# Kernel optimization log

Measured on AMD Instinct MI355X. Metric: run time of the kernel, lower is better.

The kernel has to match this reference:

```python
import jax, jax.numpy as jnp
import numpy as np

N, E, H, D, L = 50000, 800000, 4, 128, 4
HD = H * D  # 512
NEG_SLOPE_ATTN = 0.2   # DGL GATConv leaky_relu on attention logits
NEG_SLOPE_ACT = 0.01   # F.leaky_relu activation on output
LN_EPS = 1e-5

def _leaky(x, s):
    return jnp.where(x > 0, x, s * x)

def setup_inputs() -> dict:
    key = jax.random.key(0)
    ks = jax.random.split(key, 12)
    features = jax.random.normal(ks[0], (N, D), dtype=jnp.float32)
    src = jax.random.randint(ks[1], (E,), 0, N, dtype=jnp.int32)
    dst = jax.random.randint(ks[2], (E,), 0, N, dtype=jnp.int32)
    s = 0.05
    W_fc   = jax.random.normal(ks[3], (L, D, HD), dtype=jnp.float32) * s
    attn_l = jax.random.normal(ks[4], (L, H, D), dtype=jnp.float32) * s
    attn_r = jax.random.normal(ks[5], (L, H, D), dtype=jnp.float32) * s
    W_res  = jax.random.normal(ks[6], (L, D, HD), dtype=jnp.float32) * s
    b_gat  = jnp.zeros((L, HD), dtype=jnp.float32)
    W_nrm  = jax.random.normal(ks[7], (L, HD, D), dtype=jnp.float32) * s
    b_nrm  = jnp.zeros((L, D), dtype=jnp.float32)
    ln_g   = jnp.ones((L, D), dtype=jnp.float32)
    ln_b   = jnp.zeros((L, D), dtype=jnp.float32)
    return dict(features=features, src=src, dst=dst, W_fc=W_fc, attn_l=attn_l,
                attn_r=attn_r, W_res=W_res, b_gat=b_gat, W_nrm=W_nrm,
                b_nrm=b_nrm, ln_g=ln_g, ln_b=ln_b)

def _gat_layer(x, src, dst, Wf, al, ar, Wr, b):
    feat = (x @ Wf).reshape(N, H, D)                      # [N,H,D]
    el = jnp.einsum('nhd,hd->nh', feat, al)               # [N,H]
    er = jnp.einsum('nhd,hd->nh', feat, ar)
    e = _leaky(el[src] + er[dst], NEG_SLOPE_ATTN)         # [E,H]
    m = jax.ops.segment_max(e, dst, num_segments=N)       # segment softmax over in-edges
    ex = jnp.exp(e - m[dst])
    z = jax.ops.segment_sum(ex, dst, num_segments=N)
    alpha = ex / jnp.maximum(z[dst], 1e-20)               # [E,H]
    msg = feat[src] * alpha[:, :, None]                   # [E,H,D] (dominant traffic)
    rst = jax.ops.segment_sum(msg, dst, num_segments=N)   # [N,H,D]
    rst = rst + (x @ Wr).reshape(N, H, D)                 # linear residual
    rst = rst + b.reshape(H, D)
    rst = _leaky(rst, NEG_SLOPE_ACT)                      # activation
    return rst.reshape(N, HD)

def _layernorm(y, g, b):
    mu = jnp.mean(y, axis=-1, keepdims=True)
    var = jnp.mean(jnp.square(y - mu), axis=-1, keepdims=True)
    return (y - mu) * jax.lax.rsqrt(var + LN_EPS) * g + b

def reference(features, src, dst, W_fc, attn_l, attn_r, W_res, b_gat, W_nrm, b_nrm, ln_g, ln_b):
    x = features
    for l in range(L):
        h = _gat_layer(x, src, dst, W_fc[l], attn_l[l], attn_r[l], W_res[l], b_gat[l])
        y = h @ W_nrm[l] + b_nrm[l]
        x = _layernorm(y, ln_g[l], ln_b[l])
    return x
```

## Files before the change

kernel.cpp:

```cpp
#include <hip/hip_runtime.h>
#include <math.h>

#define NN 50000
#define NPAD 50048
#define EE 800000
#define HH 4
#define DD 128
#define HDIM 512
#define LL 4

typedef __attribute__((ext_vector_type(8))) short short8;
typedef __attribute__((ext_vector_type(4))) float f32x4;

__device__ __forceinline__ float lk(float x, float s){ return x > 0.f ? x : s*x; }
__device__ __forceinline__ unsigned short f2bf(float f){
  unsigned u = __float_as_uint(f);
  u += 0x7FFFu + ((u >> 16) & 1u);
  return (unsigned short)(u >> 16);
}
__device__ __forceinline__ float lo16(unsigned u){ return __uint_as_float(u << 16); }
__device__ __forceinline__ float hi16(unsigned u){ return __uint_as_float(u & 0xFFFF0000u); }

__global__ void k_zero(int* p, int n){ int i = blockIdx.x*blockDim.x+threadIdx.x; if(i<n) p[i]=0; }

__global__ void k_hist(const int* __restrict__ dst, int* __restrict__ cnt){
  int e = blockIdx.x*blockDim.x+threadIdx.x;
  if (e < EE) atomicAdd(&cnt[dst[e]], 1);
}

__global__ __launch_bounds__(1024) void k_scan(const int* __restrict__ cnt, int* __restrict__ row_ptr){
  __shared__ int part[1024];
  int t = threadIdx.x;
  const int chunk = (NN + 1023)/1024;
  int b = t*chunk, e = b+chunk;
  if (b > NN) b = NN;
  if (e > NN) e = NN;
  int s = 0;
  for (int i=b;i<e;++i) s += cnt[i];
  part[t] = s;
  __syncthreads();
  for (int off=1; off<1024; off<<=1){
    int v = (t>=off) ? part[t-off] : 0;
    __syncthreads();
    part[t] += v;
    __syncthreads();
  }
  int run = part[t] - s;
  for (int i=b;i<e;++i){ row_ptr[i] = run; run += cnt[i]; }
  if (t==1023) row_ptr[NN] = part[1023];
}

__global__ void k_copy(const int* __restrict__ a, int* __restrict__ b, int n){
  int i = blockIdx.x*blockDim.x+threadIdx.x; if(i<n) b[i]=a[i];
}

__global__ void k_fill(const int* __restrict__ src, const int* __restrict__ dst,
                       int* __restrict__ cursor, int* __restrict__ csr_src){
  int e = blockIdx.x*blockDim.x+threadIdx.x;
  if (e >= EE) return;
  int d = dst[e];
  int p = atomicAdd(&cursor[d], 1);
  csr_src[p] = src[e];
}

__global__ __launch_bounds__(256) void k_cvtw2(const float* __restrict__ Wf,
                                               const float* __restrict__ Wr,
                                               unsigned short* __restrict__ W2t){
  __shared__ float tile[64][65];
  int t = threadIdx.x;
  int n0 = blockIdx.x*64, k0 = blockIdx.y*64, l = blockIdx.z;
  const float* srcp = (n0 < 512) ? Wf : Wr;
  int nsrc = (n0 < 512) ? n0 : (n0 - 512);
  #pragma unroll
  for (int j=0;j<16;++j){
    int idx = t + j*256; int kk = idx>>6, nn = idx&63;
    tile[kk][nn] = srcp[(size_t)(l*128 + k0+kk)*512 + nsrc+nn];
  }
  __syncthreads();
  #pragma unroll
  for (int j=0;j<16;++j){
    int idx = t + j*256; int nn = idx>>6, kk = idx&63;
    W2t[((size_t)l*1024 + n0+nn)*128 + k0+kk] = f2bf(tile[kk][nn]);
  }
}
__global__ __launch_bounds__(256) void k_cvtwn(const float* __restrict__ Wn,
                                               unsigned short* __restrict__ Wnt){
  __shared__ float tile[64][65];
  int t = threadIdx.x;
  int n0 = blockIdx.x*64, k0 = blockIdx.y*64, l = blockIdx.z;
  #pragma unroll
  for (int j=0;j<16;++j){
    int idx = t + j*256; int kk = idx>>6, nn = idx&63;
    tile[kk][nn] = Wn[(size_t)(l*512 + k0+kk)*128 + n0+nn];
  }
  __syncthreads();
  #pragma unroll
  for (int j=0;j<16;++j){
    int idx = t + j*256; int nn = idx>>6, kk = idx&63;
    Wnt[((size_t)l*128 + n0+nn)*512 + k0+kk] = f2bf(tile[kk][nn]);
  }
}
__global__ void k_cvtx(const float* __restrict__ x, unsigned short* __restrict__ xb){
  int idx = blockIdx.x*blockDim.x + threadIdx.x;
  int row = idx >> 7;
  xb[idx] = (row < NN) ? f2bf(x[idx]) : (unsigned short)0;
}

__global__ __launch_bounds__(256) void k_gemm1m(const unsigned short* __restrict__ xb,
                                                const unsigned short* __restrict__ W2t,
                                                const float* __restrict__ al,
                                                const float* __restrict__ ar,
                                                unsigned char* __restrict__ featQ,
                                                unsigned short* __restrict__ hbuf,
                                                float2* __restrict__ elsc,
                                                float* __restrict__ erp){
  __shared__ __attribute__((aligned(16))) char smem[2*128*136*2];
  __shared__ float sAl[128], sAr[128];
  __shared__ float sInv[128];
  unsigned short* sA = (unsigned short*)smem;
  unsigned short* sB = sA + 128*136;
  int t = threadIdx.x;
  int m0 = blockIdx.x*128;
  int n0 = blockIdx.y*128;
  int h = n0 >> 7;
  if (n0 < 512 && t < 128){ sAl[t] = al[h*128 + t]; sAr[t] = ar[h*128 + t]; }
  #pragma unroll
  for (int j=0;j<8;++j){
    int c = t + j*256; int r = c>>4, kc = c&15;
    uint4 v = *(const uint4*)(xb + (size_t)(m0+r)*128 + kc*8);
    *(uint4*)(sA + r*136 + kc*8) = v;
  }
  #pragma unroll
  for (int j=0;j<8;++j){
    int c = t + j*256; int r = c>>4, kc = c&15;
    uint4 v = *(const uint4*)(W2t + (size_t)(n0+r)*128 + kc*8);
    *(uint4*)(sB + r*136 + kc*8) = v;
  }
  __syncthreads();

  int lane = t & 63, w = t >> 6;
  int wm = (w & 1)*64, wn = (w >> 1)*64;
  int lrow = lane & 15, quad = lane >> 4;
  f32x4 acc[4][4];
  #pragma unroll
  for (int mt=0;mt<4;++mt)
    #pragma unroll
    for (int nt=0;nt<4;++nt) acc[mt][nt] = (f32x4){0.f,0.f,0.f,0.f};

  #pragma unroll
  for (int kq=0;kq<4;++kq){
    int kb = kq*32 + quad*8;
    short8 af[4], bf[4];
    #pragma unroll
    for (int mt=0;mt<4;++mt) af[mt] = *(const short8*)(sA + (wm+mt*16+lrow)*136 + kb);
    #pragma unroll
    for (int nt=0;nt<4;++nt) bf[nt] = *(const short8*)(sB + (wn+nt*16+lrow)*136 + kb);
    #pragma unroll
    for (int mt=0;mt<4;++mt)
      #pragma unroll
      for (int nt=0;nt<4;++nt)
        acc[mt][nt] = __builtin_amdgcn_mfma_f32_16x16x32_bf16(af[mt], bf[nt], acc[mt][nt], 0,0,0);
  }

  __syncthreads();
  #pragma unroll
  for (int mt=0;mt<4;++mt)
    #pragma unroll
    for (int nt=0;nt<4;++nt)
      #pragma unroll
      for (int r=0;r<4;++r)
        sA[(wm+mt*16+quad*4+r)*136 + wn+nt*16+lrow] = f2bf(acc[mt][nt][r]);
  __syncthreads();

  if (n0 >= 512){
    unsigned short* dstB = hbuf + (size_t)m0*512 + (n0-512);
    #pragma unroll
    for (int j=0;j<8;++j){
      int c = t + j*256; int r = c>>4, kc = c&15;
      uint4 v = *(const uint4*)(sA + r*136 + kc*8);
      *(uint4*)(dstB + (size_t)r*512 + kc*8) = v;
    }
  } else {
    int r = t >> 1, half = t & 1;
    int base = half*64;
    float accl = 0.f, accr = 0.f, amax = 0.f;
    #pragma unroll
    for (int d=0; d<64; d+=4){
      uint2 u = *(const uint2*)&sA[r*136 + base + d];
      float f0=lo16(u.x), f1=hi16(u.x), f2=lo16(u.y), f3=hi16(u.y);
      float4 a  = *(const float4*)&sAl[base+d];
      float4 rr = *(const float4*)&sAr[base+d];
      accl += f0*a.x + f1*a.y + f2*a.z + f3*a.w;
      accr += f0*rr.x + f1*rr.y + f2*rr.z + f3*rr.w;
      amax = fmaxf(amax, fmaxf(fmaxf(fabsf(f0), fabsf(f1)), fmaxf(fabsf(f2), fabsf(f3))));
    }
    accl += __shfl_xor(accl, 1);
    accr += __shfl_xor(accr, 1);
    amax = fmaxf(amax, __shfl_xor(amax, 1));
    float am = fmaxf(amax, 1e-8f);
    if (half == 0){
      sInv[r] = 127.f / am;
      if ((m0+r) < NN){
        elsc[(size_t)(m0+r)*4 + h] = make_float2(accl, am * (1.f/127.f));
        erp[(size_t)(m0+r)*4 + h] = accr;
      }
    }
    __syncthreads();
    float qinv = sInv[r];
    unsigned char* qdst = featQ + (size_t)(m0+r)*512 + n0 + base;
    #pragma unroll
    for (int g=0; g<4; ++g){
      uint4 ua = *(const uint4*)&sA[r*136 + base + g*16];
      uint4 ub = *(const uint4*)&sA[r*136 + base + g*16 + 8];
      unsigned vals[8] = {ua.x, ua.y, ua.z, ua.w, ub.x, ub.y, ub.z, ub.w};
      unsigned p[4];
      #pragma unroll
      for (int j=0;j<4;++j){
        unsigned vlo = vals[2*j], vhi = vals[2*j+1];
        int q0 = (int)rintf(lo16(vlo)*qinv) + 128;
        int q1 = (int)rintf(hi16(vlo)*qinv) + 128;
        int q2 = (int)rintf(lo16(vhi)*qinv) + 128;
        int q3 = (int)rintf(hi16(vhi)*qinv) + 128;
        p[j] = (unsigned)q0 | ((unsigned)q1<<8) | ((unsigned)q2<<16) | ((unsigned)q3<<24);
      }
      *(uint4*)(qdst + g*16) = make_uint4(p[0],p[1],p[2],p[3]);
    }
  }
}

__global__ __launch_bounds__(256) void k_agg(const unsigned char* __restrict__ featQ,
                                             unsigned short* __restrict__ hbuf,
                                             const float2* __restrict__ elsc,
                                             const float* __restrict__ er,
                                             const int* __restrict__ row_ptr,
                                             const int* __restrict__ csr_src,
                                             const float* __restrict__ b_gat){
  int t = threadIdx.x;
  int lane = t & 63;
  int node = blockIdx.x*4 + (t>>6);
  int beg = row_ptr[node], end = row_ptr[node+1];
  int hd = lane >> 4;
  float erh = er[(size_t)node*4 + hd];

  float z = 0.f, sws = 0.f;
  float a0=0.f,a1=0.f,a2=0.f,a3=0.f,a4=0.f,a5=0.f,a6=0.f,a7=0.f;
  const uint2* fQ = (const uint2*)featQ;

  int i = beg;
  for (; i + 3 < end; i += 4){
    int s0 = csr_src[i], s1 = csr_src[i+1], s2 = csr_src[i+2], s3 = csr_src[i+3];
    float2 q0 = elsc[(size_t)s0*4 + hd];
    float2 q1 = elsc[(size_t)s1*4 + hd];
    float2 q2 = elsc[(size_t)s2*4 + hd];
    float2 q3 = elsc[(size_t)s3*4 + hd];
    uint2 f0 = fQ[(size_t)s0*64 + lane];
    uint2 f1 = fQ[(size_t)s1*64 + lane];
    uint2 f2 = fQ[(size_t)s2*64 + lane];
    uint2 f3 = fQ[(size_t)s3*64 + lane];
    float w0 = __expf(lk(q0.x + erh, 0.2f));
    float w1 = __expf(lk(q1.x + erh, 0.2f));
    float w2 = __expf(lk(q2.x + erh, 0.2f));
    float w3 = __expf(lk(q3.x + erh, 0.2f));
    float ws0 = w0*q0.y, ws1 = w1*q1.y, ws2 = w2*q2.y, ws3 = w3*q3.y;
    z += w0 + w1 + w2 + w3;
    sws += ws0 + ws1 + ws2 + ws3;
    a0 += ws0*(float)(f0.x & 255u)      + ws1*(float)(f1.x & 255u)      + ws2*(float)(f2.x & 255u)      + ws3*(float)(f3.x & 255u);
    a1 += ws0*(float)((f0.x>>8) & 255u) + ws1*(float)((f1.x>>8) & 255u) + ws2*(float)((f2.x>>8) & 255u) + ws3*(float)((f3.x>>8) & 255u);
    a2 += ws0*(float)((f0.x>>16)& 255u) + ws1*(float)((f1.x>>16)& 255u) + ws2*(float)((f2.x>>16)& 255u) + ws3*(float)((f3.x>>16)& 255u);
    a3 += ws0*(float)(f0.x>>24)         + ws1*(float)(f1.x>>24)         + ws2*(float)(f2.x>>24)         + ws3*(float)(f3.x>>24);
    a4 += ws0*(float)(f0.y & 255u)      + ws1*(float)(f1.y & 255u)      + ws2*(float)(f2.y & 255u)      + ws3*(float)(f3.y & 255u);
    a5 += ws0*(float)((f0.y>>8) & 255u) + ws1*(float)((f1.y>>8) & 255u) + ws2*(float)((f2.y>>8) & 255u) + ws3*(float)((f3.y>>8) & 255u);
    a6 += ws0*(float)((f0.y>>16)& 255u) + ws1*(float)((f1.y>>16)& 255u) + ws2*(float)((f2.y>>16)& 255u) + ws3*(float)((f3.y>>16)& 255u);
    a7 += ws0*(float)(f0.y>>24)         + ws1*(float)(f1.y>>24)         + ws2*(float)(f2.y>>24)         + ws3*(float)(f3.y>>24);
  }
  for (; i < end; ++i){
    int s = csr_src[i];
    float2 q = elsc[(size_t)s*4 + hd];
    uint2 f = fQ[(size_t)s*64 + lane];
    float w = __expf(lk(q.x + erh, 0.2f));
    float ws = w*q.y;
    z += w; sws += ws;
    a0 += ws*(float)(f.x & 255u);       a1 += ws*(float)((f.x>>8) & 255u);
    a2 += ws*(float)((f.x>>16) & 255u); a3 += ws*(float)(f.x>>24);
    a4 += ws*(float)(f.y & 255u);       a5 += ws*(float)((f.y>>8) & 255u);
    a6 += ws*(float)((f.y>>16) & 255u); a7 += ws*(float)(f.y>>24);
  }
  float iz = 1.f / fmaxf(z, 1e-20f);
  float off = 128.f * sws;

  uint4* rp = (uint4*)(hbuf + (size_t)node*HDIM) + lane;
  uint4 rv = *rp;
  const float4* bp = (const float4*)b_gat;
  float4 b1 = bp[2*lane], b2 = bp[2*lane+1];
  float o0 = lk((a0-off)*iz + lo16(rv.x) + b1.x, 0.01f);
  float o1 = lk((a1-off)*iz + hi16(rv.x) + b1.y, 0.01f);
  float o2 = lk((a2-off)*iz + lo16(rv.y) + b1.z, 0.01f);
  float o3 = lk((a3-off)*iz + hi16(rv.y) + b1.w, 0.01f);
  float o4 = lk((a4-off)*iz + lo16(rv.z) + b2.x, 0.01f);
  float o5 = lk((a5-off)*iz + hi16(rv.z) + b2.y, 0.01f);
  float o6 = lk((a6-off)*iz + lo16(rv.w) + b2.z, 0.01f);
  float o7 = lk((a7-off)*iz + hi16(rv.w) + b2.w, 0.01f);
  uint4 wv;
  wv.x = (unsigned)f2bf(o0) | ((unsigned)f2bf(o1) << 16);
  wv.y = (unsigned)f2bf(o2) | ((unsigned)f2bf(o3) << 16);
  wv.z = (unsigned)f2bf(o4) | ((unsigned)f2bf(o5) << 16);
  wv.w = (unsigned)f2bf(o6) | ((unsigned)f2bf(o7) << 16);
  *rp = wv;
}

__global__ __launch_bounds__(256) void k_gemm3m(const unsigned short* __restrict__ h,
                                                const unsigned short* __restrict__ Wnt,
                                                const float* __restrict__ bn,
                                                const float* __restrict__ lng,
                                                const float* __restrict__ lnb,
                                                float* __restrict__ out,
                                                unsigned short* __restrict__ xb,
                                                int writeOut){
  __shared__ __attribute__((aligned(16))) char smem[2*128*136*2];
  unsigned short* sA = (unsigned short*)smem;
  unsigned short* sB = sA + 128*136;
  float* yf = (float*)smem;
  int t = threadIdx.x;
  int m0 = blockIdx.x*128;
  int lane = t & 63, w = t >> 6;
  int wm = (w & 1)*64, wn = (w >> 1)*64;
  int lrow = lane & 15, quad = lane >> 4;

  f32x4 acc[4][4];
  #pragma unroll
  for (int mt=0;mt<4;++mt)
    #pragma unroll
    for (int nt=0;nt<4;++nt) acc[mt][nt] = (f32x4){0.f,0.f,0.f,0.f};

  for (int kc2=0; kc2<4; ++kc2){
    if (kc2) __syncthreads();
    #pragma unroll
    for (int j=0;j<8;++j){
      int c = t + j*256; int r = c>>4, kc = c&15;
      uint4 v = *(const uint4*)(h + (size_t)(m0+r)*512 + kc2*128 + kc*8);
      *(uint4*)(sA + r*136 + kc*8) = v;
    }
    #pragma unroll
    for (int j=0;j<8;++j){
      int c = t + j*256; int r = c>>4, kc = c&15;
      uint4 v = *(const uint4*)(Wnt + (size_t)r*512 + kc2*128 + kc*8);
      *(uint4*)(sB + r*136 + kc*8) = v;
    }
    __syncthreads();
    #pragma unroll
    for (int kq=0;kq<4;++kq){
      int kb = kq*32 + quad*8;
      short8 af[4], bf[4];
      #pragma unroll
      for (int mt=0;mt<4;++mt) af[mt] = *(const short8*)(sA + (wm+mt*16+lrow)*136 + kb);
      #pragma unroll
      for (int nt=0;nt<4;++nt) bf[nt] = *(const short8*)(sB + (wn+nt*16+lrow)*136 + kb);
      #pragma unroll
      for (int mt=0;mt<4;++mt)
        #pragma unroll
        for (int nt=0;nt<4;++nt)
          acc[mt][nt] = __builtin_amdgcn_mfma_f32_16x16x32_bf16(af[mt], bf[nt], acc[mt][nt], 0,0,0);
    }
  }

  float bnv[4];
  #pragma unroll
  for (int nt=0;nt<4;++nt) bnv[nt] = bn[wn + nt*16 + lrow];
  __syncthreads();
  #pragma unroll
  for (int mt=0;mt<4;++mt)
    #pragma unroll
    for (int nt=0;nt<4;++nt)
      #pragma unroll
      for (int r=0;r<4;++r)
        yf[(wm+mt*16+quad*4+r)*132 + wn+nt*16+lrow] = acc[mt][nt][r] + bnv[nt];
  __syncthreads();

  float g0 = lng[lane], g1 = lng[64+lane];
  float bb0 = lnb[lane], bb1 = lnb[64+lane];
  for (int rr = w*32; rr < w*32+32; ++rr){
    float v0 = yf[rr*132 + lane], v1 = yf[rr*132 + 64 + lane];
    float s = v0 + v1;
    #pragma unroll
    for (int off=32; off>0; off>>=1) s += __shfl_xor(s, off);
    float mu = s * (1.f/128.f);
    float d0 = v0-mu, d1 = v1-mu;
    float q = d0*d0 + d1*d1;
    #pragma unroll
    for (int off=32; off>0; off>>=1) q += __shfl_xor(q, off);
    float inv = rsqrtf(q*(1.f/128.f) + 1e-5f);
    int grow = m0 + rr;
    if (grow < NN){
      float o0 = d0*inv*g0 + bb0;
      float o1 = d1*inv*g1 + bb1;
      xb[(size_t)grow*128 + lane]      = f2bf(o0);
      xb[(size_t)grow*128 + 64 + lane] = f2bf(o1);
      if (writeOut){
        out[(size_t)grow*128 + lane]      = o0;
        out[(size_t)grow*128 + 64 + lane] = o1;
      }
    }
  }
}

extern "C" void kernel_launch(void* const* d_in, const int* in_sizes, int n_in,
                              void* d_out, int out_size, void* d_ws, size_t ws_size,
                              hipStream_t stream){
  const float* features = (const float*)d_in[0];
  const int*   src      = (const int*)d_in[1];
  const int*   dst      = (const int*)d_in[2];
  const float* W_fc     = (const float*)d_in[3];
  const float* attn_l   = (const float*)d_in[4];
  const float* attn_r   = (const float*)d_in[5];
  const float* W_res    = (const float*)d_in[6];
  const float* b_gat    = (const float*)d_in[7];
  const float* W_nrm    = (const float*)d_in[8];
  const float* b_nrm    = (const float*)d_in[9];
  const float* ln_g     = (const float*)d_in[10];
  const float* ln_b     = (const float*)d_in[11];
  float* out = (float*)d_out;

  unsigned short* xb    = (unsigned short*)d_ws;
  unsigned short* hbuf  = xb + (size_t)NPAD*128;
  unsigned short* W2t   = hbuf + (size_t)NPAD*512;
  unsigned short* Wnt   = W2t + (size_t)LL*1024*128;
  unsigned char* featQ  = (unsigned char*)(Wnt + (size_t)LL*128*512);
  float2* elsc = (float2*)(featQ + (size_t)NPAD*512);
  float* er = (float*)(elsc + (size_t)NN*4);
  int* row_ptr = (int*)(er + (size_t)NN*4);
  int* cursor  = row_ptr + (NN+1);
  int* csr_src = cursor + NN;

  k_cvtw2<<<dim3(16, 2, LL), 256, 0, stream>>>(W_fc, W_res, W2t);
  k_cvtwn<<<dim3(2, 8, LL), 256, 0, stream>>>(W_nrm, Wnt);
  k_cvtx<<<(NPAD*128)/256, 256, 0, stream>>>(features, xb);
  k_zero<<<(NN+255)/256, 256, 0, stream>>>(cursor, NN);
  k_hist<<<(EE+255)/256, 256, 0, stream>>>(dst, cursor);
  k_scan<<<1, 1024, 0, stream>>>(cursor, row_ptr);
  k_copy<<<(NN+255)/256, 256, 0, stream>>>(row_ptr, cursor, NN);
  k_fill<<<(EE+255)/256, 256, 0, stream>>>(src, dst, cursor, csr_src);

  for (int l=0; l<LL; ++l){
    const unsigned short* W2l = W2t + (size_t)l*1024*128;
    const unsigned short* Wnl = Wnt + (size_t)l*128*512;
    const float* al = attn_l + (size_t)l*HH*DD;
    const float* ar = attn_r + (size_t)l*HH*DD;
    const float* bg = b_gat  + (size_t)l*HDIM;
    const float* bn = b_nrm  + (size_t)l*DD;
    const float* lg = ln_g   + (size_t)l*DD;
    const float* lb = ln_b   + (size_t)l*DD;

    k_gemm1m<<<dim3(NPAD/128, 8), 256, 0, stream>>>(xb, W2l, al, ar, featQ, hbuf, elsc, er);
    k_agg<<<NN/4, 256, 0, stream>>>(featQ, hbuf, elsc, er, row_ptr, csr_src, bg);
    k_gemm3m<<<NPAD/128, 256, 0, stream>>>(hbuf, Wnl, bn, lg, lb, out, xb, (l==LL-1) ? 1 : 0);
  }
}
```

Before: 870.5 us.

## Reuse staged X tile across four N-blocks and read weights directly from global

The first GEMM now launches 2 column groups instead of 8, with each block looping over four 128-wide output slices. This reuses one staged X tile in LDS instead of reloading it per slice. Weight fragments in both GEMMs are now read straight from global/L2 into registers instead of being staged through shared memory, which removes the B-tile LDS copy and shrinks LDS use. The trade-offs are less parallelism per launch, serialized slices per block, and possibly poorer coalescing and latency on the weight reads, which no longer go through LDS.

```diff
diff --git a/kernel.cpp b/kernel.cpp
--- a/kernel.cpp
+++ b/kernel.cpp
@@ -114,116 +114,114 @@
                                                 unsigned short* __restrict__ hbuf,
                                                 float2* __restrict__ elsc,
                                                 float* __restrict__ erp){
-  __shared__ __attribute__((aligned(16))) char smem[2*128*136*2];
-  __shared__ float sAl[128], sAr[128];
-  __shared__ float sInv[128];
-  unsigned short* sA = (unsigned short*)smem;
-  unsigned short* sB = sA + 128*136;
+  __shared__ __attribute__((aligned(16))) unsigned short sA[128*136];
+  __shared__ __attribute__((aligned(16))) unsigned short sC[128*136];
+  __shared__ float sAl[512], sAr[512], sInv[128];
   int t = threadIdx.x;
   int m0 = blockIdx.x*128;
-  int n0 = blockIdx.y*128;
-  int h = n0 >> 7;
-  if (n0 < 512 && t < 128){ sAl[t] = al[h*128 + t]; sAr[t] = ar[h*128 + t]; }
+  int isRes = blockIdx.y;
+  if (!isRes){
+    sAl[t] = al[t]; sAl[256+t] = al[256+t];
+    sAr[t] = ar[t]; sAr[256+t] = ar[256+t];
+  }
   #pragma unroll
   for (int j=0;j<8;++j){
     int c = t + j*256; int r = c>>4, kc = c&15;
     uint4 v = *(const uint4*)(xb + (size_t)(m0+r)*128 + kc*8);
     *(uint4*)(sA + r*136 + kc*8) = v;
   }
-  #pragma unroll
-  for (int j=0;j<8;++j){
-    int c = t + j*256; int r = c>>4, kc = c&15;
-    uint4 v = *(const uint4*)(W2t + (size_t)(n0+r)*128 + kc*8);
-    *(uint4*)(sB + r*136 + kc*8) = v;
-  }
   __syncthreads();
 
   int lane = t & 63, w = t >> 6;
   int wm = (w & 1)*64, wn = (w >> 1)*64;
   int lrow = lane & 15, quad = lane >> 4;
-  f32x4 acc[4][4];
-  #pragma unroll
-  for (int mt=0;mt<4;++mt)
-    #pragma unroll
-    for (int nt=0;nt<4;++nt) acc[mt][nt] = (f32x4){0.f,0.f,0.f,0.f};
-
-  #pragma unroll
-  for (int kq=0;kq<4;++kq){
-    int kb = kq*32 + quad*8;
-    short8 af[4], bf[4];
-    #pragma unroll
-    for (int mt=0;mt<4;++mt) af[mt] = *(const short8*)(sA + (wm+mt*16+lrow)*136 + kb);
-    #pragma unroll
-    for (int nt=0;nt<4;++nt) bf[nt] = *(const short8*)(sB + (wn+nt*16+lrow)*136 + kb);
+
+  for (int nb=0; nb<4; ++nb){
+    int n0 = isRes*512 + nb*128;
+    const unsigned short* Bb = W2t + (size_t)n0*128;
+    f32x4 acc[4][4];
     #pragma unroll
     for (int mt=0;mt<4;++mt)
       #pragma unroll
+      for (int nt=0;nt<4;++nt) acc[mt][nt] = (f32x4){0.f,0.f,0.f,0.f};
+
+    #pragma unroll
+    for (int kq=0;kq<4;++kq){
+      int kb = kq*32 + quad*8;
+      short8 af[4], bf[4];
+      #pragma unroll
+      for (int mt=0;mt<4;++mt) af[mt] = *(const short8*)(sA + (wm+mt*16+lrow)*136 + kb);
+      #pragma unroll
+      for (int nt=0;nt<4;++nt) bf[nt] = *(const short8*)(Bb + (size_t)(wn+nt*16+lrow)*128 + kb);
+      #pragma unroll
+      for (int mt=0;mt<4;++mt)
+        #pragma unroll
+        for (int nt=0;nt<4;++nt)
+          acc[mt][nt] = __builtin_amdgcn_mfma_f32_16x16x32_bf16(af[mt], bf[nt], acc[mt][nt], 0,0,0);
+    }
+
+    __syncthreads();
+    #pragma unroll
+    for (int mt=0;mt<4;++mt)
+      #pragma unroll
       for (int nt=0;nt<4;++nt)
-        acc[mt][nt] = __builtin_amdgcn_mfma_f32_16x16x32_bf16(af[mt], bf[nt], acc[mt][nt], 0,0,0);
-  }
-
-  __syncthreads();
-  #pragma unroll
-  for (int mt=0;mt<4;++mt)
-    #pragma unroll
-    for (int nt=0;nt<4;++nt)
-      #pragma unroll
-      for (int r=0;r<4;++r)
-        sA[(wm+mt*16+quad*4+r)*136 + wn+nt*16+lrow] = f2bf(acc[mt][nt][r]);
-  __syncthreads();
-
-  if (n0 >= 512){
-    unsigned short* dstB = hbuf + (size_t)m0*512 + (n0-512);
-    #pragma unroll
-    for (int j=0;j<8;++j){
-      int c = t + j*256; int r = c>>4, kc = c&15;
-      uint4 v = *(const uint4*)(sA + r*136 + kc*8);
-      *(uint4*)(dstB + (size_t)r*512 + kc*8) = v;
-    }
-  } else {
-    int r = t >> 1, half = t & 1;
-    int base = half*64;
-    float accl = 0.f, accr = 0.f, amax = 0.f;
-    #pragma unroll
-    for (int d=0; d<64; d+=4){
-      uint2 u = *(const uint2*)&sA[r*136 + base + d];
-      float f0=lo16(u.x), f1=hi16(u.x), f2=lo16(u.y), f3=hi16(u.y);
-      float4 a  = *(const float4*)&sAl[base+d];
-      float4 rr = *(const float4*)&sAr[base+d];
-      accl += f0*a.x + f1*a.y + f2*a.z + f3*a.w;
-      accr += f0*rr.x + f1*rr.y + f2*rr.z + f3*rr.w;
-      amax = fmaxf(amax, fmaxf(fmaxf(fabsf(f0), fabsf(f1)), fmaxf(fabsf(f2), fabsf(f3))));
-    }
-    accl += __shfl_xor(accl, 1);
-    accr += __shfl_xor(accr, 1);
-    amax = fmaxf(amax, __shfl_xor(amax, 1));
-    float am = fmaxf(amax, 1e-8f);
-    if (half == 0){
-      sInv[r] = 127.f / am;
-      if ((m0+r) < NN){
-        elsc[(size_t)(m0+r)*4 + h] = make_float2(accl, am * (1.f/127.f));
-        erp[(size_t)(m0+r)*4 + h] = accr;
+        #pragma unroll
+        for (int r=0;r<4;++r)
+          sC[(wm+mt*16+quad*4+r)*136 + wn+nt*16+lrow] = f2bf(acc[mt][nt][r]);
+    __syncthreads();
+
+    if (isRes){
+      #pragma unroll
+      for (int j=0;j<8;++j){
+        int c = t + j*256; int r = c>>4, kc = c&15;
+        uint4 v = *(const uint4*)(sC + r*136 + kc*8);
+        *(uint4*)(hbuf + (size_t)(m0+r)*512 + nb*128 + kc*8) = v;
       }
-    }
-    __syncthreads();
-    float qinv = sInv[r];
-    unsigned char* qdst = featQ + (size_t)(m0+r)*512 + n0 + base;
-    #pragma unroll
-    for (int g=0; g<4; ++g){
-      uint4 ua = *(const uint4*)&sA[r*136 + base + g*16];
-      uint4 ub = *(const uint4*)&sA[r*136 + base + g*16 + 8];
-      unsigned vals[8] = {ua.x, ua.y, ua.z, ua.w, ub.x, ub.y, ub.z, ub.w};
-      unsigned p[4];
-      #pragma unroll
-      for (int j=0;j<4;++j){
-        unsigned vlo = vals[2*j], vhi = vals[2*j+1];
-        int q0 = (int)rintf(lo16(vlo)*qinv) + 128;
-        int q1 = (int)rintf(hi16(vlo)*qinv) + 128;
-        int q2 = (int)rintf(lo16(vhi)*qinv) + 128;
-        int q3 = (int)rintf(hi16(vhi)*qinv) + 128;
-        p[j] = (unsigned)q0 | ((unsigned)q1<<8) | ((unsigned)q2<<16) | ((unsigned)q3<<24);
+    } else {
+      int r = t >> 1, half = t & 1;
+      int base = half*64;
+      float accl = 0.f, accr = 0.f, amax = 0.f;
+      #pragma unroll
+      for (int d=0; d<64; d+=4){
+        uint2 u = *(const uint2*)&sC[r*136 + base + d];
+        float f0=lo16(u.x), f1=hi16(u.x), f2=lo16(u.y), f3=hi16(u.y);
+        float4 a  = *(const float4*)&sAl[nb*128 + base + d];
+        float4 rr = *(const float4*)&sAr[nb*128 + base + d];
+        accl += f0*a.x + f1*a.y + f2*a.z + f3*a.w;
+        accr += f0*rr.x + f1*rr.y + f2*rr.z + f3*rr.w;
+        amax = fmaxf(amax, fmaxf(fmaxf(fabsf(f0), fabsf(f1)), fmaxf(fabsf(f2), fabsf(f3))));
       }
-      *(uint4*)(qdst + g*16) = make_uint4(p[0],p[1],p[2],p[3]);
+      accl += __shfl_xor(accl, 1);
+      accr += __shfl_xor(accr, 1);
+      amax = fmaxf(amax, __shfl_xor(amax, 1));
+      float am = fmaxf(amax, 1e-8f);
+      if (half == 0){
+        sInv[r] = 127.f / am;
+        if ((m0+r) < NN){
+          elsc[(size_t)(m0+r)*4 + nb] = make_float2(accl, am * (1.f/127.f));
+          erp[(size_t)(m0+r)*4 + nb] = accr;
+        }
+      }
+      __syncthreads();
+      float qinv = sInv[r];
+      unsigned char* qdst = featQ + (size_t)(m0+r)*512 + nb*128 + base;
+      #pragma unroll
+      for (int g=0; g<4; ++g){
+        uint4 ua = *(const uint4*)&sC[r*136 + base + g*16];
+        uint4 ub = *(const uint4*)&sC[r*136 + base + g*16 + 8];
+        unsigned vals[8] = {ua.x, ua.y, ua.z, ua.w, ub.x, ub.y, ub.z, ub.w};
+        unsigned p[4];
+        #pragma unroll
+        for (int j=0;j<4;++j){
+          unsigned vlo = vals[2*j], vhi = vals[2*j+1];
+          int q0 = (int)rintf(lo16(vlo)*qinv) + 128;
+          int q1 = (int)rintf(hi16(vlo)*qinv) + 128;
+          int q2 = (int)rintf(lo16(vhi)*qinv) + 128;
+          int q3 = (int)rintf(hi16(vhi)*qinv) + 128;
+          p[j] = (unsigned)q0 | ((unsigned)q1<<8) | ((unsigned)q2<<16) | ((unsigned)q3<<24);
+        }
+        *(uint4*)(qdst + g*16) = make_uint4(p[0],p[1],p[2],p[3]);
+      }
     }
   }
 }
@@ -316,9 +314,8 @@
                                                 float* __restrict__ out,
                                                 unsigned short* __restrict__ xb,
                                                 int writeOut){
-  __shared__ __attribute__((aligned(16))) char smem[2*128*136*2];
+  __shared__ __attribute__((aligned(16))) char smem[128*136*2 < 128*132*4 ? 128*132*4 : 128*136*2];
   unsigned short* sA = (unsigned short*)smem;
-  unsigned short* sB = sA + 128*136;
   float* yf = (float*)smem;
   int t = threadIdx.x;
   int m0 = blockIdx.x*128;
@@ -340,12 +337,6 @@
       uint4 v = *(const uint4*)(h + (size_t)(m0+r)*512 + kc2*128 + kc*8);
       *(uint4*)(sA + r*136 + kc*8) = v;
     }
-    #pragma unroll
-    for (int j=0;j<8;++j){
-      int c = t + j*256; int r = c>>4, kc = c&15;
-      uint4 v = *(const uint4*)(Wnt + (size_t)r*512 + kc2*128 + kc*8);
-      *(uint4*)(sB + r*136 + kc*8) = v;
-    }
     __syncthreads();
     #pragma unroll
     for (int kq=0;kq<4;++kq){
@@ -354,7 +345,7 @@
       #pragma unroll
       for (int mt=0;mt<4;++mt) af[mt] = *(const short8*)(sA + (wm+mt*16+lrow)*136 + kb);
       #pragma unroll
-      for (int nt=0;nt<4;++nt) bf[nt] = *(const short8*)(sB + (wn+nt*16+lrow)*136 + kb);
+      for (int nt=0;nt<4;++nt) bf[nt] = *(const short8*)(Wnt + (size_t)(wn+nt*16+lrow)*512 + kc2*128 + kb);
       #pragma unroll
       for (int mt=0;mt<4;++mt)
         #pragma unroll
@@ -450,7 +441,7 @@
     const float* lg = ln_g   + (size_t)l*DD;
     const float* lb = ln_b   + (size_t)l*DD;
 
-    k_gemm1m<<<dim3(NPAD/128, 8), 256, 0, stream>>>(xb, W2l, al, ar, featQ, hbuf, elsc, er);
+    k_gemm1m<<<dim3(NPAD/128, 2), 256, 0, stream>>>(xb, W2l, al, ar, featQ, hbuf, elsc, er);
     k_agg<<<NN/4, 256, 0, stream>>>(featQ, hbuf, elsc, er, row_ptr, csr_src, bg);
     k_gemm3m<<<NPAD/128, 256, 0, stream>>>(hbuf, Wnl, bn, lg, lb, out, xb, (l==LL-1) ? 1 : 0);
   }
```

New measurement: 937.2 us. +7.7%, slower.
